# Kernel optimization log

Hardware: AMD Instinct MI355X
Metric: run time of the kernel (lower is better)

Reference implementation:

```python
import jax, jax.numpy as jnp
import numpy as np

KEY_DIM = 128
TEMPERATURE = float(np.sqrt(KEY_DIM))


def setup_inputs() -> dict:
    key = jax.random.key(0)
    kq, kk, kv = jax.random.split(key, 3)
    B, S, D = 32, 2048, KEY_DIM
    q = jax.random.normal(kq, (B, S, D), dtype=jnp.float32)
    k = jax.random.normal(kk, (B, S, D), dtype=jnp.float32)
    v = jax.random.normal(kv, (B, S, D), dtype=jnp.float32)
    return {"q": q, "k": k, "v": v}


def reference(q, k, v):
    # energies: [B, S, S] = q @ k^T / sqrt(D)
    energies = jnp.einsum("bqd,bkd->bqk", q, k) / TEMPERATURE
    S = energies.shape[1]
    # causal mask: disallow attending to future positions (strict upper triangle)
    causal = jnp.tril(jnp.ones((S, S), dtype=bool))
    energies = jnp.where(causal[None, :, :], energies, -jnp.inf)
    attention = jax.nn.softmax(energies, axis=2)  # dropout p=0 -> identity
    context = jnp.einsum("bqk,bkd->bqd", attention, v)
    return (context, attention)
```

## Files before the change

### kernel.cpp

```cpp
#include <hip/hip_runtime.h>


#define BATCH 32
#define SEQ 2048
#define DIM 128
#define BQ 64
#define NT 32
#define NTHREADS 256
#define SCALE 0.08838834764831845f

typedef __attribute__((ext_vector_type(8))) short short8;
typedef __attribute__((ext_vector_type(4))) short short4v;
typedef __attribute__((ext_vector_type(4))) float floatx4;

#define QP 136
#define PP 72

__device__ __forceinline__ short f2bf(float x) {
  unsigned u = __builtin_bit_cast(unsigned, x);
  u += 0x7fffu + ((u >> 16) & 1u);
  return (short)(u >> 16);
}

__device__ __forceinline__ void stage_f32(const float* __restrict__ g,
                                          short* __restrict__ lds, int tid) {
  int r = tid >> 2, c0 = tid & 3;
  const float* grow = g + r * DIM;
  short* lrow = lds + r * QP;
#pragma unroll
  for (int i = 0; i < 8; ++i) {
    int dq = c0 + 4 * i;
    floatx4 val = *(const floatx4*)(grow + dq * 4);
    short4v o;
    o.x = f2bf(val.x); o.y = f2bf(val.y); o.z = f2bf(val.z); o.w = f2bf(val.w);
    *(short4v*)(lrow + dq * 4) = o;
  }
}
__device__ __forceinline__ void stage_vT_f32(const float* __restrict__ g,
                                             short* __restrict__ lds, int tid) {
  int r = tid >> 2, c0 = tid & 3;
  const float* grow = g + r * DIM;
#pragma unroll
  for (int i = 0; i < 8; ++i) {
    int dq = c0 + 4 * i;
    floatx4 val = *(const floatx4*)(grow + dq * 4);
    lds[(dq * 4 + 0) * PP + r] = f2bf(val.x);
    lds[(dq * 4 + 1) * PP + r] = f2bf(val.y);
    lds[(dq * 4 + 2) * PP + r] = f2bf(val.z);
    lds[(dq * 4 + 3) * PP + r] = f2bf(val.w);
  }
}
__device__ __forceinline__ void stage_k_bf(const short* __restrict__ src,
                                           short* __restrict__ ks, int tid) {
#pragma unroll
  for (int i = 0; i < 4; ++i) {
    int idx = tid + i * 256;
    int r = idx >> 4, g = idx & 15;
    *(short8*)(ks + r * QP + g * 8) = *(const short8*)(src + r * DIM + g * 8);
  }
}
__device__ __forceinline__ void stage_v_bf(const short* __restrict__ src,
                                           short* __restrict__ vts, int tid) {
#pragma unroll
  for (int i = 0; i < 4; ++i) {
    int idx = tid + i * 256;
    int d = idx >> 3, g = idx & 7;
    *(short8*)(vts + d * PP + g * 8) = *(const short8*)(src + (size_t)d * SEQ + g * 8);
  }
}

__global__ __launch_bounds__(NTHREADS) void convert_kv(
    const float* __restrict__ k, const float* __restrict__ v,
    short* __restrict__ kbf, short* __restrict__ vbf) {
  int blk = blockIdx.x, tid = threadIdx.x;
  if (blk < BATCH * NT) {
    __shared__ short vt[DIM * PP];
    int b = blk >> 5, s0 = (blk & 31) * BQ;
    const float* src = v + ((size_t)b * SEQ + s0) * DIM;
    int r = tid >> 2, c0 = tid & 3;
#pragma unroll
    for (int i = 0; i < 8; ++i) {
      int dq = c0 + 4 * i;
      floatx4 val = *(const floatx4*)(src + (size_t)r * DIM + dq * 4);
      vt[(dq * 4 + 0) * PP + r] = f2bf(val.x);
      vt[(dq * 4 + 1) * PP + r] = f2bf(val.y);
      vt[(dq * 4 + 2) * PP + r] = f2bf(val.z);
      vt[(dq * 4 + 3) * PP + r] = f2bf(val.w);
    }
    __syncthreads();
#pragma unroll
    for (int i = 0; i < 4; ++i) {
      int idx = tid + i * 256;
      int d = idx >> 3, g = idx & 7;
      *(short8*)(vbf + ((size_t)b * DIM + d) * SEQ + s0 + g * 8) =
          *(const short8*)(vt + d * PP + g * 8);
    }
  } else {
    size_t base = (size_t)(blk - BATCH * NT) * 4096;
    const floatx4* src = (const floatx4*)k;
#pragma unroll
    for (int i = 0; i < 16; ++i) {
      size_t idx = base + i * 256 + tid;
      floatx4 val = src[idx];
      short4v o;
      o.x = f2bf(val.x); o.y = f2bf(val.y); o.z = f2bf(val.z); o.w = f2bf(val.w);
      *(short4v*)(kbf + idx * 4) = o;
    }
  }
}

template <bool PRE>
__global__ __launch_bounds__(NTHREADS, 2) void attn_fused(
    const float* __restrict__ q, const float* __restrict__ k,
    const float* __restrict__ v, const short* __restrict__ kbf,
    const short* __restrict__ vbf, float* __restrict__ ctx,
    float* __restrict__ attn) {
  __shared__ short ks[BQ * QP];
  __shared__ short rest[18432];
  short* vts = rest;
  short* psA = rest + DIM * PP;
  short* psB = psA + BQ * PP;

  const int tid = threadIdx.x;
  const int i = blockIdx.x;
  const int xcd = i & 7;
  const int jj = i >> 3;
  const int b = xcd + 8 * (jj >> 4);
  const int pr = jj & 15;
  const int qtA = pr, qtB = 31 - pr;

  const float* qbase = q + (size_t)b * SEQ * DIM;
  const short* kb = PRE ? kbf + (size_t)b * SEQ * DIM : nullptr;
  const short* vb = PRE ? vbf + (size_t)b * DIM * SEQ : nullptr;
  const float* kbase = k + (size_t)b * SEQ * DIM;
  const float* vbase = v + (size_t)b * SEQ * DIM;
  float* ctxA = ctx + ((size_t)b * SEQ + qtA * BQ) * DIM;
  float* ctxB = ctx + ((size_t)b * SEQ + qtB * BQ) * DIM;
  float* attnA = attn + ((size_t)b * SEQ + qtA * BQ) * SEQ;
  float* attnB = attn + ((size_t)b * SEQ + qtB * BQ) * SEQ;

  stage_f32(qbase + (size_t)qtA * BQ * DIM, rest, tid);
  stage_f32(qbase + (size_t)qtB * BQ * DIM, rest + BQ * QP, tid);

  const int lane = tid & 63;
  const int w = tid >> 6;
  const int quad = lane >> 4;
  const int c = lane & 15;

  __syncthreads();
  short8 afA[4], afB[4];
  {
    const short* ra = rest + (w * 16 + c) * QP + quad * 8;
    const short* rb = ra + BQ * QP;
#pragma unroll
    for (int kk = 0; kk < 4; ++kk) {
      afA[kk] = *(const short8*)(ra + kk * 32);
      afB[kk] = *(const short8*)(rb + kk * 32);
    }
  }

  {
    floatx4 z4 = {0.f, 0.f, 0.f, 0.f};
    int zcA = (qtA + 1) * BQ, nzA = (SEQ - zcA) >> 2;
    for (int r = 0; r < BQ; ++r) {
      float* rowp = attnA + (size_t)r * SEQ + zcA;
      for (int c4 = tid; c4 < nzA; c4 += NTHREADS) *(floatx4*)(rowp + c4 * 4) = z4;
    }
    int zcB = (qtB + 1) * BQ, nzB = (SEQ - zcB) >> 2;
    for (int r = 0; r < BQ; ++r) {
      float* rowp = attnB + (size_t)r * SEQ + zcB;
      for (int c4 = tid; c4 < nzB; c4 += NTHREADS) *(floatx4*)(rowp + c4 * 4) = z4;
    }
  }

  const int lrow_lo = w * 16 + quad * 4;

  float plA[4] = {0.f, 0.f, 0.f, 0.f}, plB[4] = {0.f, 0.f, 0.f, 0.f};
  for (int kt = 0; kt <= qtB; ++kt) {
    __syncthreads();
    if (PRE) stage_k_bf(kb + (size_t)kt * BQ * DIM, ks, tid);
    else     stage_f32(kbase + (size_t)kt * BQ * DIM, ks, tid);
    __syncthreads();

#pragma unroll
    for (int nt = 0; nt < 4; ++nt) {
      floatx4 a = {0.f, 0.f, 0.f, 0.f};
      const short* brow = ks + (nt * 16 + c) * QP + quad * 8;
#pragma unroll
      for (int kk = 0; kk < 4; ++kk)
        a = __builtin_amdgcn_mfma_f32_16x16x32_bf16(
            afB[kk], *(const short8*)(brow + kk * 32), a, 0, 0, 0);
      bool diag = (kt == qtB);
#pragma unroll
      for (int r = 0; r < 4; ++r) {
        bool msk = diag && (nt * 16 + c > lrow_lo + r);
        plB[r] += msk ? 0.f : __expf(a[r] * SCALE);
      }
    }
    if (kt <= qtA) {
#pragma unroll
      for (int nt = 0; nt < 4; ++nt) {
        floatx4 a = {0.f, 0.f, 0.f, 0.f};
        const short* brow = ks + (nt * 16 + c) * QP + quad * 8;
#pragma unroll
        for (int kk = 0; kk < 4; ++kk)
          a = __builtin_amdgcn_mfma_f32_16x16x32_bf16(
              afA[kk], *(const short8*)(brow + kk * 32), a, 0, 0, 0);
        bool diag = (kt == qtA);
#pragma unroll
        for (int r = 0; r < 4; ++r) {
          bool msk = diag && (nt * 16 + c > lrow_lo + r);
          plA[r] += msk ? 0.f : __expf(a[r] * SCALE);
        }
      }
    }
  }
  float invlA[4], invlB[4];
#pragma unroll
  for (int r = 0; r < 4; ++r) {
#pragma unroll
    for (int off = 1; off < 16; off <<= 1) {
      plA[r] += __shfl_xor(plA[r], off, 16);
      plB[r] += __shfl_xor(plB[r], off, 16);
    }
    invlA[r] = 1.f / plA[r];
    invlB[r] = 1.f / plB[r];
  }

  floatx4 oaccA[8], oaccB[8];
#pragma unroll
  for (int nt = 0; nt < 8; ++nt) { oaccA[nt] = (floatx4)(0.f); oaccB[nt] = (floatx4)(0.f); }

  const short* prowA = psA + (w * 16 + c) * PP + quad * 8;
  const short* prowB = psB + (w * 16 + c) * PP + quad * 8;

  for (int kt = 0; kt <= qtB; ++kt) {
    __syncthreads();
    if (PRE) {
      stage_k_bf(kb + (size_t)kt * BQ * DIM, ks, tid);
      stage_v_bf(vb + (size_t)kt * BQ, vts, tid);
    } else {
      stage_f32(kbase + (size_t)kt * BQ * DIM, ks, tid);
      stage_vT_f32(vbase + (size_t)kt * BQ * DIM, vts, tid);
    }
    __syncthreads();

    const bool activeA = (kt <= qtA);
#pragma unroll
    for (int nt = 0; nt < 4; ++nt) {
      floatx4 a = {0.f, 0.f, 0.f, 0.f};
      const short* brow = ks + (nt * 16 + c) * QP + quad * 8;
#pragma unroll
      for (int kk = 0; kk < 4; ++kk)
        a = __builtin_amdgcn_mfma_f32_16x16x32_bf16(
            afB[kk], *(const short8*)(brow + kk * 32), a, 0, 0, 0);
      bool diag = (kt == qtB);
#pragma unroll
      for (int r = 0; r < 4; ++r) {
        bool msk = diag && (nt * 16 + c > lrow_lo + r);
        float p = msk ? 0.f : __expf(a[r] * SCALE) * invlB[r];
        psB[(lrow_lo + r) * PP + nt * 16 + c] = f2bf(p);
      }
    }
    if (activeA) {
#pragma unroll
      for (int nt = 0; nt < 4; ++nt) {
        floatx4 a = {0.f, 0.f, 0.f, 0.f};
        const short* brow = ks + (nt * 16 + c) * QP + quad * 8;
#pragma unroll
        for (int kk = 0; kk < 4; ++kk)
          a = __builtin_amdgcn_mfma_f32_16x16x32_bf16(
              afA[kk], *(const short8*)(brow + kk * 32), a, 0, 0, 0);
        bool diag = (kt == qtA);
#pragma unroll
        for (int r = 0; r < 4; ++r) {
          bool msk = diag && (nt * 16 + c > lrow_lo + r);
          float p = msk ? 0.f : __expf(a[r] * SCALE) * invlA[r];
          psA[(lrow_lo + r) * PP + nt * 16 + c] = f2bf(p);
        }
      }
    }
    __syncthreads();

#pragma unroll
    for (int ks2 = 0; ks2 < 2; ++ks2) {
      short8 paB = *(const short8*)(prowB + ks2 * 32);
      short8 paA;
      if (activeA) paA = *(const short8*)(prowA + ks2 * 32);
#pragma unroll
      for (int nt = 0; nt < 8; ++nt) {
        short8 vf = *(const short8*)(vts + (nt * 16 + c) * PP + ks2 * 32 + quad * 8);
        oaccB[nt] = __builtin_amdgcn_mfma_f32_16x16x32_bf16(paB, vf, oaccB[nt], 0, 0, 0);
        if (activeA)
          oaccA[nt] = __builtin_amdgcn_mfma_f32_16x16x32_bf16(paA, vf, oaccA[nt], 0, 0, 0);
      }
    }

#pragma unroll
    for (int half = 0; half < 2; ++half) {
      int idx = tid + half * 256;
      int r = idx >> 3, g = idx & 7;
      short8 pb = *(const short8*)(psB + r * PP + g * 8);
      float* dst = attnB + (size_t)r * SEQ + kt * BQ + g * 8;
      floatx4 lo, hi;
      lo.x = __builtin_bit_cast(float, (unsigned)((unsigned short)pb[0] << 16));
      lo.y = __builtin_bit_cast(float, (unsigned)((unsigned short)pb[1] << 16));
      lo.z = __builtin_bit_cast(float, (unsigned)((unsigned short)pb[2] << 16));
      lo.w = __builtin_bit_cast(float, (unsigned)((unsigned short)pb[3] << 16));
      hi.x = __builtin_bit_cast(float, (unsigned)((unsigned short)pb[4] << 16));
      hi.y = __builtin_bit_cast(float, (unsigned)((unsigned short)pb[5] << 16));
      hi.z = __builtin_bit_cast(float, (unsigned)((unsigned short)pb[6] << 16));
      hi.w = __builtin_bit_cast(float, (unsigned)((unsigned short)pb[7] << 16));
      *(floatx4*)dst = lo;
      *(floatx4*)(dst + 4) = hi;
      if (activeA) {
        short8 pa = *(const short8*)(psA + r * PP + g * 8);
        float* dstA = attnA + (size_t)r * SEQ + kt * BQ + g * 8;
        floatx4 lo2, hi2;
        lo2.x = __builtin_bit_cast(float, (unsigned)((unsigned short)pa[0] << 16));
        lo2.y = __builtin_bit_cast(float, (unsigned)((unsigned short)pa[1] << 16));
        lo2.z = __builtin_bit_cast(float, (unsigned)((unsigned short)pa[2] << 16));
        lo2.w = __builtin_bit_cast(float, (unsigned)((unsigned short)pa[3] << 16));
        hi2.x = __builtin_bit_cast(float, (unsigned)((unsigned short)pa[4] << 16));
        hi2.y = __builtin_bit_cast(float, (unsigned)((unsigned short)pa[5] << 16));
        hi2.z = __builtin_bit_cast(float, (unsigned)((unsigned short)pa[6] << 16));
        hi2.w = __builtin_bit_cast(float, (unsigned)((unsigned short)pa[7] << 16));
        *(floatx4*)dstA = lo2;
        *(floatx4*)(dstA + 4) = hi2;
      }
    }
  }

#pragma unroll
  for (int nt = 0; nt < 8; ++nt)
#pragma unroll
    for (int r = 0; r < 4; ++r) {
      ctxA[(size_t)(lrow_lo + r) * DIM + nt * 16 + c] = oaccA[nt][r];
      ctxB[(size_t)(lrow_lo + r) * DIM + nt * 16 + c] = oaccB[nt][r];
    }
}

extern "C" void kernel_launch(void* const* d_in, const int* in_sizes, int n_in,
                              void* d_out, int out_size, void* d_ws, size_t ws_size,
                              hipStream_t stream) {
  (void)in_sizes; (void)n_in; (void)out_size;
  const float* q = (const float*)d_in[0];
  const float* k = (const float*)d_in[1];
  const float* v = (const float*)d_in[2];
  float* ctx = (float*)d_out;
  float* attn = ctx + (size_t)BATCH * SEQ * DIM;
  const size_t kv_elems = (size_t)BATCH * SEQ * DIM;
  const size_t need = kv_elems * 2 * sizeof(short);
  dim3 grid(BATCH * NT / 2);
  if (ws_size >= need) {
    short* kbf = (short*)d_ws;
    short* vbf = kbf + kv_elems;
    convert_kv<<<dim3(BATCH * NT + 512), NTHREADS, 0, stream>>>(k, v, kbf, vbf);
    attn_fused<true><<<grid, NTHREADS, 0, stream>>>(q, k, v, kbf, vbf, ctx, attn);
  } else {
    attn_fused<false><<<grid, NTHREADS, 0, stream>>>(q, k, v, nullptr, nullptr, ctx, attn);
  }
}
```

Measured before the change: 749.7 us.

## Software-pipeline K/V staging, interleave zero-fill, and make P writeback warp-local

In the normalizer pass, K tiles are double-buffered in LDS (reusing the Q staging buffer) and prefetched into registers one tile ahead. The zero-fill of the masked upper triangle is spread across loop iterations so it can overlap compute. In the output pass, K/V for the next tile are prefetched into registers, the A and B score MFMAs share loaded K fragments, and attention writeback is done per-wave on its own rows, removing one barrier per iteration. This raises register pressure and relies on the rest buffer being free after Q fragments are loaded.

New measurement: 710.5 us. 5.2% less time.

```diff
diff --git a/kernel.cpp b/kernel.cpp
--- a/kernel.cpp
+++ b/kernel.cpp
@@ -21,6 +21,9 @@
   u += 0x7fffu + ((u >> 16) & 1u);
   return (short)(u >> 16);
 }
+__device__ __forceinline__ float bf2f(short s) {
+  return __builtin_bit_cast(float, (unsigned)(unsigned short)s << 16);
+}
 
 __device__ __forceinline__ void stage_f32(const float* __restrict__ g,
                                           short* __restrict__ lds, int tid) {
@@ -50,22 +53,40 @@
     lds[(dq * 4 + 3) * PP + r] = f2bf(val.w);
   }
 }
-__device__ __forceinline__ void stage_k_bf(const short* __restrict__ src,
-                                           short* __restrict__ ks, int tid) {
+__device__ __forceinline__ void load_k_regs(const short* __restrict__ src,
+                                            int tid, short8* kr) {
 #pragma unroll
   for (int i = 0; i < 4; ++i) {
     int idx = tid + i * 256;
     int r = idx >> 4, g = idx & 15;
-    *(short8*)(ks + r * QP + g * 8) = *(const short8*)(src + r * DIM + g * 8);
-  }
-}
-__device__ __forceinline__ void stage_v_bf(const short* __restrict__ src,
-                                           short* __restrict__ vts, int tid) {
+    kr[i] = *(const short8*)(src + r * DIM + g * 8);
+  }
+}
+__device__ __forceinline__ void write_k_regs(const short8* kr,
+                                             short* __restrict__ ks, int tid) {
+#pragma unroll
+  for (int i = 0; i < 4; ++i) {
+    int idx = tid + i * 256;
+    int r = idx >> 4, g = idx & 15;
+    *(short8*)(ks + r * QP + g * 8) = kr[i];
+  }
+}
+__device__ __forceinline__ void load_v_regs(const short* __restrict__ src,
+                                            int tid, short8* vr) {
 #pragma unroll
   for (int i = 0; i < 4; ++i) {
     int idx = tid + i * 256;
     int d = idx >> 3, g = idx & 7;
-    *(short8*)(vts + d * PP + g * 8) = *(const short8*)(src + (size_t)d * SEQ + g * 8);
+    vr[i] = *(const short8*)(src + (size_t)d * SEQ + g * 8);
+  }
+}
+__device__ __forceinline__ void write_v_regs(const short8* vr,
+                                             short* __restrict__ vts, int tid) {
+#pragma unroll
+  for (int i = 0; i < 4; ++i) {
+    int idx = tid + i * 256;
+    int d = idx >> 3, g = idx & 7;
+    *(short8*)(vts + d * PP + g * 8) = vr[i];
   }
 }
 
@@ -159,62 +180,75 @@
     }
   }
 
-  {
-    floatx4 z4 = {0.f, 0.f, 0.f, 0.f};
-    int zcA = (qtA + 1) * BQ, nzA = (SEQ - zcA) >> 2;
-    for (int r = 0; r < BQ; ++r) {
-      float* rowp = attnA + (size_t)r * SEQ + zcA;
-      for (int c4 = tid; c4 < nzA; c4 += NTHREADS) *(floatx4*)(rowp + c4 * 4) = z4;
-    }
-    int zcB = (qtB + 1) * BQ, nzB = (SEQ - zcB) >> 2;
-    for (int r = 0; r < BQ; ++r) {
-      float* rowp = attnB + (size_t)r * SEQ + zcB;
-      for (int c4 = tid; c4 < nzB; c4 += NTHREADS) *(floatx4*)(rowp + c4 * 4) = z4;
-    }
-  }
-
   const int lrow_lo = w * 16 + quad * 4;
+  const int nIt = qtB + 1;
+  const int zcA = (qtA + 1) * BQ, nzA4 = (SEQ - zcA) >> 2;
+  const int zcB = (qtB + 1) * BQ, nzB4 = (SEQ - zcB) >> 2;
+  const floatx4 z4 = {0.f, 0.f, 0.f, 0.f};
 
   float plA[4] = {0.f, 0.f, 0.f, 0.f}, plB[4] = {0.f, 0.f, 0.f, 0.f};
-  for (int kt = 0; kt <= qtB; ++kt) {
+  if (PRE) {
+    short8 kr[4];
+    load_k_regs(kb, tid, kr);
+    write_k_regs(kr, ks, tid);
+  } else {
+    stage_f32(kbase, ks, tid);
+  }
+  __syncthreads();
+  for (int kt = 0; kt < nIt; ++kt) {
+    short* cur = (kt & 1) ? rest : ks;
+    short* nxt = (kt & 1) ? ks : rest;
+    const bool more = (kt + 1 < nIt);
+    short8 kr[4];
+    if (PRE && more) load_k_regs(kb + (size_t)(kt + 1) * BQ * DIM, tid, kr);
+
+    const bool activeA = (kt <= qtA);
+    const bool diagB = (kt == qtB), diagA = (kt == qtA);
+#pragma unroll
+    for (int nt = 0; nt < 4; ++nt) {
+      const short* brow = cur + (nt * 16 + c) * QP + quad * 8;
+      short8 bf[4];
+#pragma unroll
+      for (int kk = 0; kk < 4; ++kk) bf[kk] = *(const short8*)(brow + kk * 32);
+      floatx4 aB = {0.f, 0.f, 0.f, 0.f};
+#pragma unroll
+      for (int kk = 0; kk < 4; ++kk)
+        aB = __builtin_amdgcn_mfma_f32_16x16x32_bf16(afB[kk], bf[kk], aB, 0, 0, 0);
+#pragma unroll
+      for (int r = 0; r < 4; ++r) {
+        bool msk = diagB && (nt * 16 + c > lrow_lo + r);
+        plB[r] += msk ? 0.f : __expf(aB[r] * SCALE);
+      }
+      if (activeA) {
+        floatx4 aA = {0.f, 0.f, 0.f, 0.f};
+#pragma unroll
+        for (int kk = 0; kk < 4; ++kk)
+          aA = __builtin_amdgcn_mfma_f32_16x16x32_bf16(afA[kk], bf[kk], aA, 0, 0, 0);
+#pragma unroll
+        for (int r = 0; r < 4; ++r) {
+          bool msk = diagA && (nt * 16 + c > lrow_lo + r);
+          plA[r] += msk ? 0.f : __expf(aA[r] * SCALE);
+        }
+      }
+    }
+
+    {
+      int r0 = (kt * BQ) / nIt, r1 = ((kt + 1) * BQ) / nIt;
+      for (int r = r0; r < r1; ++r) {
+        float* rowpA = attnA + (size_t)r * SEQ + zcA;
+        for (int c4 = tid; c4 < nzA4; c4 += NTHREADS) *(floatx4*)(rowpA + c4 * 4) = z4;
+        float* rowpB = attnB + (size_t)r * SEQ + zcB;
+        for (int c4 = tid; c4 < nzB4; c4 += NTHREADS) *(floatx4*)(rowpB + c4 * 4) = z4;
+      }
+    }
+
+    if (more) {
+      if (PRE) write_k_regs(kr, nxt, tid);
+      else stage_f32(kbase + (size_t)(kt + 1) * BQ * DIM, nxt, tid);
+    }
     __syncthreads();
-    if (PRE) stage_k_bf(kb + (size_t)kt * BQ * DIM, ks, tid);
-    else     stage_f32(kbase + (size_t)kt * BQ * DIM, ks, tid);
-    __syncthreads();
-
-#pragma unroll
-    for (int nt = 0; nt < 4; ++nt) {
-      floatx4 a = {0.f, 0.f, 0.f, 0.f};
-      const short* brow = ks + (nt * 16 + c) * QP + quad * 8;
-#pragma unroll
-      for (int kk = 0; kk < 4; ++kk)
-        a = __builtin_amdgcn_mfma_f32_16x16x32_bf16(
-            afB[kk], *(const short8*)(brow + kk * 32), a, 0, 0, 0);
-      bool diag = (kt == qtB);
-#pragma unroll
-      for (int r = 0; r < 4; ++r) {
-        bool msk = diag && (nt * 16 + c > lrow_lo + r);
-        plB[r] += msk ? 0.f : __expf(a[r] * SCALE);
-      }
-    }
-    if (kt <= qtA) {
-#pragma unroll
-      for (int nt = 0; nt < 4; ++nt) {
-        floatx4 a = {0.f, 0.f, 0.f, 0.f};
-        const short* brow = ks + (nt * 16 + c) * QP + quad * 8;
-#pragma unroll
-        for (int kk = 0; kk < 4; ++kk)
-          a = __builtin_amdgcn_mfma_f32_16x16x32_bf16(
-              afA[kk], *(const short8*)(brow + kk * 32), a, 0, 0, 0);
-        bool diag = (kt == qtA);
-#pragma unroll
-        for (int r = 0; r < 4; ++r) {
-          bool msk = diag && (nt * 16 + c > lrow_lo + r);
-          plA[r] += msk ? 0.f : __expf(a[r] * SCALE);
-        }
-      }
-    }
-  }
+  }
+
   float invlA[4], invlB[4];
 #pragma unroll
   for (int r = 0; r < 4; ++r) {
@@ -234,53 +268,55 @@
   const short* prowA = psA + (w * 16 + c) * PP + quad * 8;
   const short* prowB = psB + (w * 16 + c) * PP + quad * 8;
 
-  for (int kt = 0; kt <= qtB; ++kt) {
+  short8 kr2[4], vr2[4];
+  if (PRE) { load_k_regs(kb, tid, kr2); load_v_regs(vb, tid, vr2); }
+  for (int kt = 0; kt < nIt; ++kt) {
     __syncthreads();
     if (PRE) {
-      stage_k_bf(kb + (size_t)kt * BQ * DIM, ks, tid);
-      stage_v_bf(vb + (size_t)kt * BQ, vts, tid);
+      write_k_regs(kr2, ks, tid);
+      write_v_regs(vr2, vts, tid);
     } else {
       stage_f32(kbase + (size_t)kt * BQ * DIM, ks, tid);
       stage_vT_f32(vbase + (size_t)kt * BQ * DIM, vts, tid);
     }
     __syncthreads();
+    const bool more = (kt + 1 < nIt);
+    if (PRE && more) {
+      load_k_regs(kb + (size_t)(kt + 1) * BQ * DIM, tid, kr2);
+      load_v_regs(vb + (size_t)(kt + 1) * BQ, tid, vr2);
+    }
 
     const bool activeA = (kt <= qtA);
+    const bool diagB = (kt == qtB), diagA = (kt == qtA);
 #pragma unroll
     for (int nt = 0; nt < 4; ++nt) {
-      floatx4 a = {0.f, 0.f, 0.f, 0.f};
       const short* brow = ks + (nt * 16 + c) * QP + quad * 8;
+      short8 bf[4];
+#pragma unroll
+      for (int kk = 0; kk < 4; ++kk) bf[kk] = *(const short8*)(brow + kk * 32);
+      floatx4 aB = {0.f, 0.f, 0.f, 0.f};
 #pragma unroll
       for (int kk = 0; kk < 4; ++kk)
-        a = __builtin_amdgcn_mfma_f32_16x16x32_bf16(
-            afB[kk], *(const short8*)(brow + kk * 32), a, 0, 0, 0);
-      bool diag = (kt == qtB);
+        aB = __builtin_amdgcn_mfma_f32_16x16x32_bf16(afB[kk], bf[kk], aB, 0, 0, 0);
 #pragma unroll
       for (int r = 0; r < 4; ++r) {
-        bool msk = diag && (nt * 16 + c > lrow_lo + r);
-        float p = msk ? 0.f : __expf(a[r] * SCALE) * invlB[r];
+        bool msk = diagB && (nt * 16 + c > lrow_lo + r);
+        float p = msk ? 0.f : __expf(aB[r] * SCALE) * invlB[r];
         psB[(lrow_lo + r) * PP + nt * 16 + c] = f2bf(p);
       }
-    }
-    if (activeA) {
-#pragma unroll
-      for (int nt = 0; nt < 4; ++nt) {
-        floatx4 a = {0.f, 0.f, 0.f, 0.f};
-        const short* brow = ks + (nt * 16 + c) * QP + quad * 8;
+      if (activeA) {
+        floatx4 aA = {0.f, 0.f, 0.f, 0.f};
 #pragma unroll
         for (int kk = 0; kk < 4; ++kk)
-          a = __builtin_amdgcn_mfma_f32_16x16x32_bf16(
-              afA[kk], *(const short8*)(brow + kk * 32), a, 0, 0, 0);
-        bool diag = (kt == qtA);
+          aA = __builtin_amdgcn_mfma_f32_16x16x32_bf16(afA[kk], bf[kk], aA, 0, 0, 0);
 #pragma unroll
         for (int r = 0; r < 4; ++r) {
-          bool msk = diag && (nt * 16 + c > lrow_lo + r);
-          float p = msk ? 0.f : __expf(a[r] * SCALE) * invlA[r];
+          bool msk = diagA && (nt * 16 + c > lrow_lo + r);
+          float p = msk ? 0.f : __expf(aA[r] * SCALE) * invlA[r];
           psA[(lrow_lo + r) * PP + nt * 16 + c] = f2bf(p);
         }
       }
     }
-    __syncthreads();
 
 #pragma unroll
     for (int ks2 = 0; ks2 < 2; ++ks2) {
@@ -297,36 +333,19 @@
     }
 
 #pragma unroll
-    for (int half = 0; half < 2; ++half) {
-      int idx = tid + half * 256;
-      int r = idx >> 3, g = idx & 7;
-      short8 pb = *(const short8*)(psB + r * PP + g * 8);
-      float* dst = attnB + (size_t)r * SEQ + kt * BQ + g * 8;
-      floatx4 lo, hi;
-      lo.x = __builtin_bit_cast(float, (unsigned)((unsigned short)pb[0] << 16));
-      lo.y = __builtin_bit_cast(float, (unsigned)((unsigned short)pb[1] << 16));
-      lo.z = __builtin_bit_cast(float, (unsigned)((unsigned short)pb[2] << 16));
-      lo.w = __builtin_bit_cast(float, (unsigned)((unsigned short)pb[3] << 16));
-      hi.x = __builtin_bit_cast(float, (unsigned)((unsigned short)pb[4] << 16));
-      hi.y = __builtin_bit_cast(float, (unsigned)((unsigned short)pb[5] << 16));
-      hi.z = __builtin_bit_cast(float, (unsigned)((unsigned short)pb[6] << 16));
-      hi.w = __builtin_bit_cast(float, (unsigned)((unsigned short)pb[7] << 16));
-      *(floatx4*)dst = lo;
-      *(floatx4*)(dst + 4) = hi;
+    for (int it = 0; it < 4; ++it) {
+      int idx = lane + it * 64;
+      int r = (idx >> 4) + w * 16;
+      int q4 = idx & 15;
+      short4v pb = *(const short4v*)(psB + r * PP + q4 * 4);
+      floatx4 fo;
+      fo.x = bf2f(pb.x); fo.y = bf2f(pb.y); fo.z = bf2f(pb.z); fo.w = bf2f(pb.w);
+      *(floatx4*)(attnB + (size_t)r * SEQ + kt * BQ + q4 * 4) = fo;
       if (activeA) {
-        short8 pa = *(const short8*)(psA + r * PP + g * 8);
-        float* dstA = attnA + (size_t)r * SEQ + kt * BQ + g * 8;
-        floatx4 lo2, hi2;
-        lo2.x = __builtin_bit_cast(float, (unsigned)((unsigned short)pa[0] << 16));
-        lo2.y = __builtin_bit_cast(float, (unsigned)((unsigned short)pa[1] << 16));
-        lo2.z = __builtin_bit_cast(float, (unsigned)((unsigned short)pa[2] << 16));
-        lo2.w = __builtin_bit_cast(float, (unsigned)((unsigned short)pa[3] << 16));
-        hi2.x = __builtin_bit_cast(float, (unsigned)((unsigned short)pa[4] << 16));
-        hi2.y = __builtin_bit_cast(float, (unsigned)((unsigned short)pa[5] << 16));
-        hi2.z = __builtin_bit_cast(float, (unsigned)((unsigned short)pa[6] << 16));
-        hi2.w = __builtin_bit_cast(float, (unsigned)((unsigned short)pa[7] << 16));
-        *(floatx4*)dstA = lo2;
-        *(floatx4*)(dstA + 4) = hi2;
+        short4v pa = *(const short4v*)(psA + r * PP + q4 * 4);
+        floatx4 fa;
+        fa.x = bf2f(pa.x); fa.y = bf2f(pa.y); fa.z = bf2f(pa.z); fa.w = bf2f(pa.w);
+        *(floatx4*)(attnA + (size_t)r * SEQ + kt * BQ + q4 * 4) = fa;
       }
     }
   }
```
